# Optimization experiments

Hardware: AMD Instinct MI355X
Metric: run time of the kernel (lower is better)

Reference implementation:

```python
import jax, jax.numpy as jnp
import numpy as np

K = 7          # kernel_size (window)
PAD = (K - 1) // 2  # SAME padding for stride 1


def setup_inputs() -> dict:
    key = jax.random.key(0)
    ks = jax.random.split(key, 7)
    B, H, W, C, F = 8, 128, 128, 256, 256
    rs = F // 2  # rel_size
    return {
        "x": jax.random.normal(ks[0], (B, H, W, C), jnp.float32),
        "Wq": jax.random.normal(ks[1], (C, F), jnp.float32) * 0.05,
        "Wk": jax.random.normal(ks[2], (C, F), jnp.float32) * 0.05,
        "Wv": jax.random.normal(ks[3], (C, F), jnp.float32) * 0.05,
        "rel_x": jax.random.normal(ks[4], (rs, K), jnp.float32) * 0.05,
        "rel_y": jax.random.normal(ks[5], (F - rs, K), jnp.float32) * 0.05,
        "bias": jax.random.normal(ks[6], (1, 1, 1, F), jnp.float32) * (1.0 / np.sqrt(F).astype(np.float32)),
    }


def reference(x, Wq, Wk, Wv, rel_x, rel_y, bias):
    B, H, W, C = x.shape
    rs = rel_x.shape[0]
    # 1x1 conv projections (single group)
    q = jnp.einsum('bhwc,cf->bhwf', x, Wq)
    k = jnp.einsum('bhwc,cf->bhwf', x, Wk)
    v = jnp.einsum('bhwc,cf->bhwf', x, Wv)
    kp = jnp.pad(k, ((0, 0), (PAD, PAD), (PAD, PAD), (0, 0)))
    vp = jnp.pad(v, ((0, 0), (PAD, PAD), (PAD, PAD), (0, 0)))
    # window scores: sum_c q * shifted(k) -> [b,h,w,kh,kw]; avoids im2col blowup
    scores = jnp.stack([
        jnp.stack([jnp.einsum('bhwf,bhwf->bhw', q, kp[:, i:i + H, j:j + W, :])
                   for j in range(K)], axis=-1)
        for i in range(K)], axis=-2)
    # relative position terms: x-half broadcasts along rows (kh), y-half along cols (kw)
    qx = jnp.einsum('bhwx,xk->bhwk', q[..., :rs], rel_x)
    qy = jnp.einsum('bhwy,yk->bhwk', q[..., rs:], rel_y)
    scores = scores + qx[:, :, :, None, :] + qy[:, :, :, :, None]
    attn = jax.nn.softmax(scores.reshape(B, H, W, K * K), axis=-1).reshape(B, H, W, K, K)
    # attention-weighted sum over the window for each channel
    out = sum(attn[:, :, :, i, j][..., None] * vp[:, i:i + H, j:j + W, :]
              for i in range(K) for j in range(K))
    return out + bias
```

## Files before the change

### kernel.cpp

```cpp
#include <hip/hip_runtime.h>
#include <hip/hip_fp16.h>
#include <stdint.h>

typedef _Float16 half8 __attribute__((ext_vector_type(8)));
typedef _Float16 half2v __attribute__((ext_vector_type(2)));
typedef __attribute__((ext_vector_type(4))) float f32x4;

__device__ __forceinline__ unsigned short f2h(float f) {
  __half h = __float2half(f);
  unsigned short u; __builtin_memcpy(&u, &h, 2); return u;
}
__device__ __forceinline__ unsigned pk2h(float a, float b) {
  auto v = __builtin_amdgcn_cvt_pkrtz(a, b);
  unsigned u; __builtin_memcpy(&u, &v, 4); return u;
}
__device__ __forceinline__ half2v h2cast(unsigned u) {
  half2v v; __builtin_memcpy(&v, &u, 4); return v;
}

#if __has_builtin(__builtin_amdgcn_fdot2)
__device__ __forceinline__ float dot2(half2v a, half2v b, float c) {
  return __builtin_amdgcn_fdot2(a, b, c, false);
}
#else
__device__ __forceinline__ float dot2(half2v a, half2v b, float c) {
  return c + (float)a[0] * (float)b[0] + (float)a[1] * (float)b[1];
}
#endif

__device__ __forceinline__ void gl_lds16(const void* g, void* l) {
  __builtin_amdgcn_global_load_lds(
      (const __attribute__((address_space(1))) void*)g,
      (__attribute__((address_space(3))) void*)l, 16, 0, 0);
}

__global__ __launch_bounds__(256) void prep(const float* __restrict__ x,
                                            const float* __restrict__ Wq,
                                            const float* __restrict__ Wk,
                                            const float* __restrict__ Wv,
                                            unsigned short* __restrict__ xh,
                                            unsigned short* __restrict__ Wb) {
  const int bid = blockIdx.x;
  if (bid < 16384) {
    const size_t i = ((size_t)bid * 256 + threadIdx.x) * 8;
    float4 a = *(const float4*)&x[i];
    float4 b = *(const float4*)&x[i + 4];
    uint4 o;
    o.x = pk2h(a.x, a.y); o.y = pk2h(a.z, a.w);
    o.z = pk2h(b.x, b.y); o.w = pk2h(b.z, b.w);
    *(uint4*)&xh[i] = o;
  } else {
    const int e = bid - 16384;
    const int w = e >> 8;
    const int n = e & 255;
    const float* W = (w == 0) ? Wq : ((w == 1) ? Wk : Wv);
    const int k = threadIdx.x;
    Wb[(size_t)e * 256 + k] = f2h(W[(size_t)k * 256 + n]);
  }
}

__global__ __launch_bounds__(256) void qkv_gemm(const unsigned short* __restrict__ xh,
                                                const unsigned short* __restrict__ Wb,
                                                unsigned short* __restrict__ qkv) {
  __shared__ unsigned char ldsb[32768];

  const int tid = threadIdx.x;
  const int l = tid & 63, l15 = l & 15, l4 = l >> 4;
  const int wv = tid >> 6, wr = wv >> 1, wc = wv & 1;

  const int pid = blockIdx.x;
  const int cid = (pid & 7) * 768 + (pid >> 3);
  const int by = cid / 6;
  const int bx = cid - by * 6;
  const size_t row0 = (size_t)by * 128;
  const int n0 = bx * 128;

  const int rbase0 = wv * 32, rbase1 = wv * 32 + 16;
  const int rA0 = rbase0 + (l >> 2), rA1 = rbase1 + (l >> 2);
  const int q0 = (l & 3) ^ ((rA0 >> 1) & 3), q1 = (l & 3) ^ ((rA1 >> 1) & 3);
  const unsigned short* gA0 = xh + (row0 + rA0) * 256 + q0 * 8;
  const unsigned short* gA1 = xh + (row0 + rA1) * 256 + q1 * 8;
  const unsigned short* gB0 = Wb + (size_t)(n0 + rA0) * 256 + q0 * 8;
  const unsigned short* gB1 = Wb + (size_t)(n0 + rA1) * 256 + q1 * 8;

  f32x4 acc[4][4] = {};

  auto stage = [&](int s, int d) {
    gl_lds16(gA0 + s * 32, &ldsb[d * 8192 + rbase0 * 64]);
    gl_lds16(gA1 + s * 32, &ldsb[d * 8192 + rbase1 * 64]);
    gl_lds16(gB0 + s * 32, &ldsb[16384 + d * 8192 + rbase0 * 64]);
    gl_lds16(gB1 + s * 32, &ldsb[16384 + d * 8192 + rbase1 * 64]);
  };

  stage(0, 0);
  __syncthreads();

  for (int s = 0; s < 8; ++s) {
    const int d = s & 1;
    if (s < 7) stage(s + 1, d ^ 1);
    half8 af[4], bf[4];
#pragma unroll
    for (int m = 0; m < 4; ++m) {
      const int r = wr * 64 + m * 16 + l15;
      af[m] = *(const half8*)&ldsb[d * 8192 + r * 64 + ((l4 ^ ((r >> 1) & 3)) * 16)];
    }
#pragma unroll
    for (int n = 0; n < 4; ++n) {
      const int r = wc * 64 + n * 16 + l15;
      bf[n] = *(const half8*)&ldsb[16384 + d * 8192 + r * 64 + ((l4 ^ ((r >> 1) & 3)) * 16)];
    }
#pragma unroll
    for (int n = 0; n < 4; ++n)
#pragma unroll
      for (int m = 0; m < 4; ++m)
        acc[m][n] = __builtin_amdgcn_mfma_f32_16x16x32_f16(af[m], bf[n], acc[m][n], 0, 0, 0);
    __syncthreads();
  }

#pragma unroll
  for (int m = 0; m < 4; ++m)
#pragma unroll
    for (int n = 0; n < 4; ++n) {
      const int ng = n0 + wc * 64 + n * 16 + l15;
      unsigned short* op = qkv + (size_t)(ng >> 8) * 33554432 + (ng & 255);
#pragma unroll
      for (int r = 0; r < 4; ++r) {
        const size_t grow = row0 + wr * 64 + m * 16 + l4 * 4 + r;
        op[grow * 256] = f2h(acc[m][n][r]);
      }
    }
}

__global__ __launch_bounds__(256) void qrel(const unsigned short* __restrict__ q,
                                            const float* __restrict__ relx,
                                            const float* __restrict__ rely,
                                            unsigned short* __restrict__ qr) {
  __shared__ unsigned wpk[896];
  for (int i = threadIdx.x; i < 896; i += 256) {
    const int hf = (i >= 448) ? 1 : 0;
    const int r = i - hf * 448;
    const int c2 = r / 7, j = r - c2 * 7;
    const float* R = hf ? rely : relx;
    wpk[i] = pk2h(R[(2 * c2) * 7 + j], R[(2 * c2 + 1) * 7 + j]);
  }
  __syncthreads();
  const size_t pix = (size_t)blockIdx.x * 256 + threadIdx.x;
  const uint4* qp = (const uint4*)(q + pix * 256);
  float ax[7] = {0, 0, 0, 0, 0, 0, 0}, ay[7] = {0, 0, 0, 0, 0, 0, 0};
#pragma unroll
  for (int g = 0; g < 32; ++g) {
    const uint4 u = qp[g];
    const int c2b = (g & 15) * 4;
    if (g < 16) {
#pragma unroll
      for (int j = 0; j < 7; ++j) {
        float s = ax[j];
        s = dot2(h2cast(u.x), h2cast(wpk[(c2b + 0) * 7 + j]), s);
        s = dot2(h2cast(u.y), h2cast(wpk[(c2b + 1) * 7 + j]), s);
        s = dot2(h2cast(u.z), h2cast(wpk[(c2b + 2) * 7 + j]), s);
        s = dot2(h2cast(u.w), h2cast(wpk[(c2b + 3) * 7 + j]), s);
        ax[j] = s;
      }
    } else {
#pragma unroll
      for (int j = 0; j < 7; ++j) {
        float s = ay[j];
        s = dot2(h2cast(u.x), h2cast(wpk[448 + (c2b + 0) * 7 + j]), s);
        s = dot2(h2cast(u.y), h2cast(wpk[448 + (c2b + 1) * 7 + j]), s);
        s = dot2(h2cast(u.z), h2cast(wpk[448 + (c2b + 2) * 7 + j]), s);
        s = dot2(h2cast(u.w), h2cast(wpk[448 + (c2b + 3) * 7 + j]), s);
        ay[j] = s;
      }
    }
  }
  uint4 o0, o1;
  o0.x = pk2h(ax[0], ax[1]); o0.y = pk2h(ax[2], ax[3]);
  o0.z = pk2h(ax[4], ax[5]); o0.w = pk2h(ax[6], ay[0]);
  o1.x = pk2h(ay[1], ay[2]); o1.y = pk2h(ay[3], ay[4]);
  o1.z = pk2h(ay[5], ay[6]); o1.w = 0;
  uint4* dst = (uint4*)(qr + pix * 512);
  dst[0] = o0; dst[1] = o1;
}

__global__ __launch_bounds__(512, 2) void attn(const unsigned short* __restrict__ qkv,
                                               const float* __restrict__ bias,
                                               const unsigned short* __restrict__ qrelb,
                                               float* __restrict__ out) {
  __shared__ unsigned short kv[2][4][4256];

  const int tid = threadIdx.x;
  const int px = tid & 255;
  const int ph = tid >> 8;
  const int col = px & 31, row = px >> 5;
  const int wv = tid >> 6;
  const int lo = tid & 15, hi = (tid >> 4) & 3;
  const int rp = wv >> 1;
  const int ch16 = (wv & 1) * 16;

  const int pid = blockIdx.x;
  const int cid = (pid & 7) * 64 + (pid >> 3);
  const int ht = cid & 15, wt = (cid >> 4) & 3, b = cid >> 6;

  const int h = ht * 8 + row, w = wt * 32 + col;
  const size_t pix = (size_t)((b * 128 + h) * 128 + w);
  const int pbase = row * 38 + col;

  const unsigned short* qb = qkv;
  const unsigned short* kb = qkv + 33554432;
  const unsigned short* vb = qkv + 67108864;

  const int pr0 = tid / 38, pc0 = tid - pr0 * 38;
  const int gh0 = ht * 8 + pr0 - 3, gw0 = wt * 32 + pc0 - 3;
  const bool ok0 = ((unsigned)gh0 < 128u) && ((unsigned)gw0 < 128u);
  const long long go0 = ((long long)((b * 128 + gh0) * 128 + gw0)) * 256;

  const int p1 = tid + 512;
  const int pr1 = p1 / 38, pc1 = p1 - pr1 * 38;
  const int gh1 = ht * 8 + pr1 - 3, gw1 = wt * 32 + pc1 - 3;
  const bool ok1 = (p1 < 532) && ((unsigned)gh1 < 128u) && ((unsigned)gw1 < 128u);
  const long long go1 = ((long long)((b * 128 + gh1) * 128 + gw1)) * 256;

  auto stage = [&](const unsigned short* base, int c, int d) {
#pragma unroll
    for (int g = 0; g < 4; ++g) {
      if (ok0) gl_lds16(base + go0 + c * 32 + g * 8, &kv[d][g][wv * 512]);
      if (ok1) gl_lds16(base + go1 + c * 32 + g * 8, &kv[d][g][4096]);
    }
  };

  auto zero_oob = [&]() {
    const uint4 z = make_uint4(0u, 0u, 0u, 0u);
    for (int p = tid; p < 532; p += 512) {
      const int pr = p / 38, pc = p - pr * 38;
      const int gh = ht * 8 + pr - 3, gw = wt * 32 + pc - 3;
      if (!((unsigned)gh < 128u && (unsigned)gw < 128u)) {
#pragma unroll
        for (int d = 0; d < 2; ++d)
#pragma unroll
          for (int g = 0; g < 4; ++g)
            *(uint4*)&kv[d][g][p * 8] = z;
      }
    }
  };

  zero_oob();
  stage(kb, 0, 0);
  __syncthreads();

  int slot0[7];
#pragma unroll
  for (int t = 0; t < 7; ++t) {
    const int p = t * 16 + lo;
    const int ur = p / 14, uc = p - ur * 14;
    slot0[t] = (2 * rp + ur) * 38 + ch16 + uc;
  }
  const size_t qpix =
      (size_t)((b * 128 + ht * 8 + 2 * rp + (lo >> 3)) * 128 + wt * 32 + ch16 + (lo & 7));
  const unsigned short* qlane = qb + qpix * 256 + hi * 8;

  f32x4 acc[2][7] = {};

  for (int s = 0; s < 8; ++s) {
    const int d = s & 1;
    if (s < 7) stage(kb, s + 1, d ^ 1);
    half8 qf[2];
#pragma unroll
    for (int g = 0; g < 2; ++g)
      qf[g] = *(const half8*)(qlane + (size_t)g * 2048 + s * 32);
    const unsigned short* kpl = &kv[d][hi][0];
    __builtin_amdgcn_s_setprio(1);
#pragma unroll
    for (int t = 0; t < 7; ++t) {
      const unsigned short* kt = kpl + slot0[t] * 8;
#pragma unroll
      for (int g = 0; g < 2; ++g) {
        const half8 kf = *(const half8*)(kt + g * 64);
        acc[g][t] = __builtin_amdgcn_mfma_f32_16x16x32_f16(qf[g], kf, acc[g][t], 0, 0, 0);
      }
    }
    __builtin_amdgcn_s_setprio(0);
    __syncthreads();
  }

  float* pbuf = (float*)&kv[0][0][0];
#pragma unroll
  for (int t = 0; t < 7; ++t) {
    const int p = t * 16 + lo;
    const int ur = p / 14, uc = p - ur * 14;
#pragma unroll
    for (int r = 0; r < 4; ++r) {
      const int q = hi * 4 + r;
      const int di = ur - (q >> 3), dj = uc - (q & 7);
      if (((unsigned)di < 7u) && ((unsigned)dj < 7u)) {
        const int pslot = di * 7 + dj;
#pragma unroll
        for (int g = 0; g < 2; ++g) {
          const int prow_ = (2 * rp + (q >> 3)) * 32 + ch16 + 8 * g + (q & 7);
          pbuf[prow_ * 52 + pslot] = acc[g][t][r];
        }
      }
    }
  }
  __syncthreads();

  float sc[49];
  {
    const float* prow = pbuf + px * 52;
#pragma unroll
    for (int k = 0; k < 12; ++k) {
      const float4 v = ((const float4*)prow)[k];
      sc[k * 4 + 0] = v.x; sc[k * 4 + 1] = v.y;
      sc[k * 4 + 2] = v.z; sc[k * 4 + 3] = v.w;
    }
    sc[48] = prow[48];
  }
  __syncthreads();

  zero_oob();
  stage(vb, 0, 0);

  float qx[7], qy[7];
  {
    const uint4* rpq = (const uint4*)(qrelb + pix * 512);
    uint4 r0 = rpq[0], r1 = rpq[1];
    half2v a0 = h2cast(r0.x), a1 = h2cast(r0.y), a2 = h2cast(r0.z), a3 = h2cast(r0.w);
    half2v b0 = h2cast(r1.x), b1 = h2cast(r1.y), b2 = h2cast(r1.z);
    qx[0] = a0[0]; qx[1] = a0[1]; qx[2] = a1[0]; qx[3] = a1[1];
    qx[4] = a2[0]; qx[5] = a2[1]; qx[6] = a3[0];
    qy[0] = a3[1]; qy[1] = b0[0]; qy[2] = b0[1]; qy[3] = b1[0];
    qy[4] = b1[1]; qy[5] = b2[0]; qy[6] = b2[1];
  }

#pragma unroll
  for (int i = 0; i < 7; ++i)
#pragma unroll
    for (int j = 0; j < 7; ++j) sc[i * 7 + j] += qx[j] + qy[i];
  float mx = sc[0];
#pragma unroll
  for (int t = 1; t < 49; ++t) mx = fmaxf(mx, sc[t]);
  float sum = 0.0f;
#pragma unroll
  for (int t = 0; t < 49; ++t) {
    float e = __expf(sc[t] - mx);
    sc[t] = e;
    sum += e;
  }
  const float invs = 1.0f / sum;
  unsigned pw[49];
#pragma unroll
  for (int t = 0; t < 49; ++t) {
    const unsigned short phv = f2h(sc[t] * invs);
    pw[t] = (unsigned)phv | ((unsigned)phv << 16);
  }
  __syncthreads();

  for (int s = 0; s < 8; ++s) {
    const int d = s & 1;
    const int f0 = s * 32 + ph * 16;
    if (s < 7) stage(vb, s + 1, d ^ 1);
    half2v acc2[8];
#pragma unroll
    for (int a = 0; a < 8; ++a) acc2[a] = half2v{(_Float16)0, (_Float16)0};
    __builtin_amdgcn_s_setprio(1);
#pragma unroll
    for (int i = 0; i < 7; ++i) {
      const int rb8 = (pbase + i * 38) * 8;
      uint4 ua[8];
#pragma unroll
      for (int j = 0; j < 4; ++j) {
        ua[2 * j + 0] = *(const uint4*)&kv[d][2 * ph + 0][rb8 + j * 8];
        ua[2 * j + 1] = *(const uint4*)&kv[d][2 * ph + 1][rb8 + j * 8];
      }
#pragma unroll
      for (int j = 0; j < 4; ++j) {
        const half2v p2h = h2cast(pw[i * 7 + j]);
        acc2[0] += p2h * h2cast(ua[2 * j + 0].x);  acc2[1] += p2h * h2cast(ua[2 * j + 0].y);
        acc2[2] += p2h * h2cast(ua[2 * j + 0].z);  acc2[3] += p2h * h2cast(ua[2 * j + 0].w);
        acc2[4] += p2h * h2cast(ua[2 * j + 1].x);  acc2[5] += p2h * h2cast(ua[2 * j + 1].y);
        acc2[6] += p2h * h2cast(ua[2 * j + 1].z);  acc2[7] += p2h * h2cast(ua[2 * j + 1].w);
      }
      uint4 ub[6];
#pragma unroll
      for (int j = 0; j < 3; ++j) {
        ub[2 * j + 0] = *(const uint4*)&kv[d][2 * ph + 0][rb8 + (j + 4) * 8];
        ub[2 * j + 1] = *(const uint4*)&kv[d][2 * ph + 1][rb8 + (j + 4) * 8];
      }
#pragma unroll
      for (int j = 0; j < 3; ++j) {
        const half2v p2h = h2cast(pw[i * 7 + 4 + j]);
        acc2[0] += p2h * h2cast(ub[2 * j + 0].x);  acc2[1] += p2h * h2cast(ub[2 * j + 0].y);
        acc2[2] += p2h * h2cast(ub[2 * j + 0].z);  acc2[3] += p2h * h2cast(ub[2 * j + 0].w);
        acc2[4] += p2h * h2cast(ub[2 * j + 1].x);  acc2[5] += p2h * h2cast(ub[2 * j + 1].y);
        acc2[6] += p2h * h2cast(ub[2 * j + 1].z);  acc2[7] += p2h * h2cast(ub[2 * j + 1].w);
      }
    }
    __builtin_amdgcn_s_setprio(0);
#pragma unroll
    for (int fq = 0; fq < 4; ++fq) {
      float4 bv = *(const float4*)&bias[f0 + fq * 4];
      float4 o;
      o.x = (float)acc2[fq * 2 + 0][0] + bv.x;
      o.y = (float)acc2[fq * 2 + 0][1] + bv.y;
      o.z = (float)acc2[fq * 2 + 1][0] + bv.z;
      o.w = (float)acc2[fq * 2 + 1][1] + bv.w;
      *(float4*)&out[pix * 256 + f0 + fq * 4] = o;
    }
    if (s < 7) __syncthreads();
  }
}

extern "C" void kernel_launch(void* const* d_in, const int* in_sizes, int n_in,
                              void* d_out, int out_size, void* d_ws, size_t ws_size,
                              hipStream_t stream) {
  const float* x = (const float*)d_in[0];
  const float* Wq = (const float*)d_in[1];
  const float* Wk = (const float*)d_in[2];
  const float* Wv = (const float*)d_in[3];
  const float* relx = (const float*)d_in[4];
  const float* rely = (const float*)d_in[5];
  const float* bias = (const float*)d_in[6];
  float* out = (float*)d_out;

  unsigned short* xh = (unsigned short*)d_out;
  unsigned short* qrl = (unsigned short*)d_out;
  unsigned short* Wb = (unsigned short*)d_ws;
  unsigned short* qkv = (unsigned short*)((char*)d_ws + 393216);

  prep<<<dim3(17152), dim3(256), 0, stream>>>(x, Wq, Wk, Wv, xh, Wb);
  qkv_gemm<<<dim3(6144), dim3(256), 0, stream>>>(xh, Wb, qkv);
  qrel<<<dim3(512), dim3(256), 0, stream>>>(qkv, relx, rely, qrl);
  attn<<<dim3(512), dim3(512), 0, stream>>>(qkv, bias, qrl, out);
}
```

Before: 273.4 us.

## Compute two vertically adjacent pixels per thread to share V window loads

Each thread now handles two pixels in adjacent rows over 8 channels, instead of one pixel over 16 channels. It loads 8 window rows of V from LDS once and feeds both pixels' accumulators, so shared-memory reads per output drop. Softmax weights for both pixels are packed into one register array. In exchange, each thread does two softmaxes serially and holds more live registers, which could hurt occupancy under the 512x2 launch bounds.

```diff
diff --git a/kernel.cpp b/kernel.cpp
--- a/kernel.cpp
+++ b/kernel.cpp
@@ -189,21 +189,24 @@
   __shared__ unsigned short kv[2][4][4256];
 
   const int tid = threadIdx.x;
-  const int px = tid & 255;
-  const int ph = tid >> 8;
-  const int col = px & 31, row = px >> 5;
   const int wv = tid >> 6;
   const int lo = tid & 15, hi = (tid >> 4) & 3;
   const int rp = wv >> 1;
   const int ch16 = (wv & 1) * 16;
 
+  const int q = tid >> 7;
+  const int pa = (tid >> 5) & 3;
+  const int pc = tid & 31;
+
   const int pid = blockIdx.x;
   const int cid = (pid & 7) * 64 + (pid >> 3);
   const int ht = cid & 15, wt = (cid >> 4) & 3, b = cid >> 6;
 
-  const int h = ht * 8 + row, w = wt * 32 + col;
-  const size_t pix = (size_t)((b * 128 + h) * 128 + w);
-  const int pbase = row * 38 + col;
+  const int hA = ht * 8 + 2 * pa, wA = wt * 32 + pc;
+  const size_t pixA = (size_t)((b * 128 + hA) * 128 + wA);
+  const size_t pixB = pixA + 128;
+  const int pxA = 2 * pa * 32 + pc;
+  const int pxB = pxA + 32;
 
   const unsigned short* qb = qkv;
   const unsigned short* kb = qkv + 33554432;
@@ -231,8 +234,8 @@
   auto zero_oob = [&]() {
     const uint4 z = make_uint4(0u, 0u, 0u, 0u);
     for (int p = tid; p < 532; p += 512) {
-      const int pr = p / 38, pc = p - pr * 38;
-      const int gh = ht * 8 + pr - 3, gw = wt * 32 + pc - 3;
+      const int pr = p / 38, pcx = p - pr * 38;
+      const int gh = ht * 8 + pr - 3, gw = wt * 32 + pcx - 3;
       if (!((unsigned)gh < 128u && (unsigned)gw < 128u)) {
 #pragma unroll
         for (int d = 0; d < 2; ++d)
@@ -289,13 +292,13 @@
     const int ur = p / 14, uc = p - ur * 14;
 #pragma unroll
     for (int r = 0; r < 4; ++r) {
-      const int q = hi * 4 + r;
-      const int di = ur - (q >> 3), dj = uc - (q & 7);
+      const int qq = hi * 4 + r;
+      const int di = ur - (qq >> 3), dj = uc - (qq & 7);
       if (((unsigned)di < 7u) && ((unsigned)dj < 7u)) {
         const int pslot = di * 7 + dj;
 #pragma unroll
         for (int g = 0; g < 2; ++g) {
-          const int prow_ = (2 * rp + (q >> 3)) * 32 + ch16 + 8 * g + (q & 7);
+          const int prow_ = (2 * rp + (qq >> 3)) * 32 + ch16 + 8 * g + (qq & 7);
           pbuf[prow_ * 52 + pslot] = acc[g][t][r];
         }
       }
@@ -303,9 +306,10 @@
   }
   __syncthreads();
 
-  float sc[49];
+  unsigned pwp[49];
   {
-    const float* prow = pbuf + px * 52;
+    float sc[49];
+    const float* prow = pbuf + pxA * 52;
 #pragma unroll
     for (int k = 0; k < 12; ++k) {
       const float4 v = ((const float4*)prow)[k];
@@ -313,97 +317,122 @@
       sc[k * 4 + 2] = v.z; sc[k * 4 + 3] = v.w;
     }
     sc[48] = prow[48];
-  }
-  __syncthreads();
-
-  zero_oob();
-  stage(vb, 0, 0);
-
-  float qx[7], qy[7];
-  {
-    const uint4* rpq = (const uint4*)(qrelb + pix * 512);
+    const uint4* rpq = (const uint4*)(qrelb + pixA * 512);
     uint4 r0 = rpq[0], r1 = rpq[1];
     half2v a0 = h2cast(r0.x), a1 = h2cast(r0.y), a2 = h2cast(r0.z), a3 = h2cast(r0.w);
     half2v b0 = h2cast(r1.x), b1 = h2cast(r1.y), b2 = h2cast(r1.z);
-    qx[0] = a0[0]; qx[1] = a0[1]; qx[2] = a1[0]; qx[3] = a1[1];
-    qx[4] = a2[0]; qx[5] = a2[1]; qx[6] = a3[0];
-    qy[0] = a3[1]; qy[1] = b0[0]; qy[2] = b0[1]; qy[3] = b1[0];
-    qy[4] = b1[1]; qy[5] = b2[0]; qy[6] = b2[1];
-  }
-
-#pragma unroll
-  for (int i = 0; i < 7; ++i)
-#pragma unroll
-    for (int j = 0; j < 7; ++j) sc[i * 7 + j] += qx[j] + qy[i];
-  float mx = sc[0];
-#pragma unroll
-  for (int t = 1; t < 49; ++t) mx = fmaxf(mx, sc[t]);
-  float sum = 0.0f;
-#pragma unroll
-  for (int t = 0; t < 49; ++t) {
-    float e = __expf(sc[t] - mx);
-    sc[t] = e;
-    sum += e;
-  }
-  const float invs = 1.0f / sum;
-  unsigned pw[49];
-#pragma unroll
-  for (int t = 0; t < 49; ++t) {
-    const unsigned short phv = f2h(sc[t] * invs);
-    pw[t] = (unsigned)phv | ((unsigned)phv << 16);
-  }
+    float qx[7] = {a0[0], a0[1], a1[0], a1[1], a2[0], a2[1], a3[0]};
+    float qy[7] = {a3[1], b0[0], b0[1], b1[0], b1[1], b2[0], b2[1]};
+#pragma unroll
+    for (int i = 0; i < 7; ++i)
+#pragma unroll
+      for (int j = 0; j < 7; ++j) sc[i * 7 + j] += qx[j] + qy[i];
+    float mx = sc[0];
+#pragma unroll
+    for (int t = 1; t < 49; ++t) mx = fmaxf(mx, sc[t]);
+    float sum = 0.0f;
+#pragma unroll
+    for (int t = 0; t < 49; ++t) {
+      float e = __expf(sc[t] - mx);
+      sc[t] = e;
+      sum += e;
+    }
+    const float invs = 1.0f / sum;
+#pragma unroll
+    for (int t = 0; t < 49; ++t) pwp[t] = (unsigned)f2h(sc[t] * invs);
+  }
+  {
+    float sc[49];
+    const float* prow = pbuf + pxB * 52;
+#pragma unroll
+    for (int k = 0; k < 12; ++k) {
+      const float4 v = ((const float4*)prow)[k];
+      sc[k * 4 + 0] = v.x; sc[k * 4 + 1] = v.y;
+      sc[k * 4 + 2] = v.z; sc[k * 4 + 3] = v.w;
+    }
+    sc[48] = prow[48];
+    const uint4* rpq = (const uint4*)(qrelb + pixB * 512);
+    uint4 r0 = rpq[0], r1 = rpq[1];
+    half2v a0 = h2cast(r0.x), a1 = h2cast(r0.y), a2 = h2cast(r0.z), a3 = h2cast(r0.w);
+    half2v b0 = h2cast(r1.x), b1 = h2cast(r1.y), b2 = h2cast(r1.z);
+    float qx[7] = {a0[0], a0[1], a1[0], a1[1], a2[0], a2[1], a3[0]};
+    float qy[7] = {a3[1], b0[0], b0[1], b1[0], b1[1], b2[0], b2[1]};
+#pragma unroll
+    for (int i = 0; i < 7; ++i)
+#pragma unroll
+      for (int j = 0; j < 7; ++j) sc[i * 7 + j] += qx[j] + qy[i];
+    float mx = sc[0];
+#pragma unroll
+    for (int t = 1; t < 49; ++t) mx = fmaxf(mx, sc[t]);
+    float sum = 0.0f;
+#pragma unroll
+    for (int t = 0; t < 49; ++t) {
+      float e = __expf(sc[t] - mx);
+      sc[t] = e;
+      sum += e;
+    }
+    const float invs = 1.0f / sum;
+#pragma unroll
+    for (int t = 0; t < 49; ++t) pwp[t] |= ((unsigned)f2h(sc[t] * invs)) << 16;
+  }
+  __syncthreads();
+
+  zero_oob();
+  stage(vb, 0, 0);
   __syncthreads();
 
   for (int s = 0; s < 8; ++s) {
     const int d = s & 1;
-    const int f0 = s * 32 + ph * 16;
+    const int f0 = s * 32 + q * 8;
     if (s < 7) stage(vb, s + 1, d ^ 1);
-    half2v acc2[8];
-#pragma unroll
-    for (int a = 0; a < 8; ++a) acc2[a] = half2v{(_Float16)0, (_Float16)0};
+    half2v accA[4], accB[4];
+#pragma unroll
+    for (int a2 = 0; a2 < 4; ++a2) {
+      accA[a2] = half2v{(_Float16)0, (_Float16)0};
+      accB[a2] = half2v{(_Float16)0, (_Float16)0};
+    }
     __builtin_amdgcn_s_setprio(1);
 #pragma unroll
-    for (int i = 0; i < 7; ++i) {
-      const int rb8 = (pbase + i * 38) * 8;
-      uint4 ua[8];
-#pragma unroll
-      for (int j = 0; j < 4; ++j) {
-        ua[2 * j + 0] = *(const uint4*)&kv[d][2 * ph + 0][rb8 + j * 8];
-        ua[2 * j + 1] = *(const uint4*)&kv[d][2 * ph + 1][rb8 + j * 8];
-      }
-#pragma unroll
-      for (int j = 0; j < 4; ++j) {
-        const half2v p2h = h2cast(pw[i * 7 + j]);
-        acc2[0] += p2h * h2cast(ua[2 * j + 0].x);  acc2[1] += p2h * h2cast(ua[2 * j + 0].y);
-        acc2[2] += p2h * h2cast(ua[2 * j + 0].z);  acc2[3] += p2h * h2cast(ua[2 * j + 0].w);
-        acc2[4] += p2h * h2cast(ua[2 * j + 1].x);  acc2[5] += p2h * h2cast(ua[2 * j + 1].y);
-        acc2[6] += p2h * h2cast(ua[2 * j + 1].z);  acc2[7] += p2h * h2cast(ua[2 * j + 1].w);
-      }
-      uint4 ub[6];
-#pragma unroll
-      for (int j = 0; j < 3; ++j) {
-        ub[2 * j + 0] = *(const uint4*)&kv[d][2 * ph + 0][rb8 + (j + 4) * 8];
-        ub[2 * j + 1] = *(const uint4*)&kv[d][2 * ph + 1][rb8 + (j + 4) * 8];
-      }
-#pragma unroll
-      for (int j = 0; j < 3; ++j) {
-        const half2v p2h = h2cast(pw[i * 7 + 4 + j]);
-        acc2[0] += p2h * h2cast(ub[2 * j + 0].x);  acc2[1] += p2h * h2cast(ub[2 * j + 0].y);
-        acc2[2] += p2h * h2cast(ub[2 * j + 0].z);  acc2[3] += p2h * h2cast(ub[2 * j + 0].w);
-        acc2[4] += p2h * h2cast(ub[2 * j + 1].x);  acc2[5] += p2h * h2cast(ub[2 * j + 1].y);
-        acc2[6] += p2h * h2cast(ub[2 * j + 1].z);  acc2[7] += p2h * h2cast(ub[2 * j + 1].w);
+    for (int u = 0; u < 8; ++u) {
+      const int rb8 = ((2 * pa + u) * 38 + pc) * 8;
+      uint4 ua[7];
+#pragma unroll
+      for (int j = 0; j < 7; ++j) ua[j] = *(const uint4*)&kv[d][q][rb8 + j * 8];
+#pragma unroll
+      for (int j = 0; j < 7; ++j) {
+        if (u < 7) {
+          const half2v pp = h2cast(pwp[u * 7 + j]);
+          const half2v p2 = half2v{pp[0], pp[0]};
+          accA[0] += p2 * h2cast(ua[j].x);
+          accA[1] += p2 * h2cast(ua[j].y);
+          accA[2] += p2 * h2cast(ua[j].z);
+          accA[3] += p2 * h2cast(ua[j].w);
+        }
+        if (u >= 1) {
+          const half2v pp = h2cast(pwp[(u - 1) * 7 + j]);
+          const half2v p2 = half2v{pp[1], pp[1]};
+          accB[0] += p2 * h2cast(ua[j].x);
+          accB[1] += p2 * h2cast(ua[j].y);
+          accB[2] += p2 * h2cast(ua[j].z);
+          accB[3] += p2 * h2cast(ua[j].w);
+        }
       }
     }
     __builtin_amdgcn_s_setprio(0);
 #pragma unroll
-    for (int fq = 0; fq < 4; ++fq) {
+    for (int fq = 0; fq < 2; ++fq) {
       float4 bv = *(const float4*)&bias[f0 + fq * 4];
-      float4 o;
-      o.x = (float)acc2[fq * 2 + 0][0] + bv.x;
-      o.y = (float)acc2[fq * 2 + 0][1] + bv.y;
-      o.z = (float)acc2[fq * 2 + 1][0] + bv.z;
-      o.w = (float)acc2[fq * 2 + 1][1] + bv.w;
-      *(float4*)&out[pix * 256 + f0 + fq * 4] = o;
+      float4 oA, oB;
+      oA.x = (float)accA[fq * 2 + 0][0] + bv.x;
+      oA.y = (float)accA[fq * 2 + 0][1] + bv.y;
+      oA.z = (float)accA[fq * 2 + 1][0] + bv.z;
+      oA.w = (float)accA[fq * 2 + 1][1] + bv.w;
+      oB.x = (float)accB[fq * 2 + 0][0] + bv.x;
+      oB.y = (float)accB[fq * 2 + 0][1] + bv.y;
+      oB.z = (float)accB[fq * 2 + 1][0] + bv.z;
+      oB.w = (float)accB[fq * 2 + 1][1] + bv.w;
+      *(float4*)&out[pixA * 256 + f0 + fq * 4] = oA;
+      *(float4*)&out[pixB * 256 + f0 + fq * 4] = oB;
     }
     if (s < 7) __syncthreads();
   }
```

Result: no change. 275.0 us (+0.6%).
